# Kernel tuning notes

Hardware: AMD Instinct MI355X
Metric: run time of the kernel (lower is better)

Reference implementation:

```python
import jax, jax.numpy as jnp
import numpy as np

N_NODES = 16000
N_EDGES = 256000
F = 128        # invariant edge feature dim
MUL = 64       # multiplicity of env/V irreps (mul_gcd)
HID = 128      # mlp_n_hidden
SQRT3 = float(np.sqrt(3.0))

# e3nn-style activation normalization constant for silu:
# c = sqrt(E_{z~N(0,1)}[silu(z)^2]), so silu(z)/c has unit second moment.
_z = np.linspace(-12.0, 12.0, 100001)
_pdf = np.exp(-0.5 * _z ** 2) / np.sqrt(2.0 * np.pi)
_silu = _z / (1.0 + np.exp(-_z))
SILU_C = float(np.sqrt(np.trapz(_silu ** 2 * _pdf, _z)))


def _nsilu(x):
    return jax.nn.silu(x) / SILU_C


def _lin(x, W):
    # e3nn 'path' gradient normalization: W ~ N(0,1), forward scaled by 1/sqrt(fan_in)
    return (x @ W) / jnp.sqrt(jnp.asarray(W.shape[0], x.dtype))


def setup_inputs() -> dict:
    key = jax.random.key(0)
    ks = jax.random.split(key, 11)
    inp = {
        'vectors': jax.random.normal(ks[0], (N_EDGES, 3), jnp.float32),
        'x': jax.random.normal(ks[1], (N_EDGES, F), jnp.float32),
        'V': jax.random.normal(ks[2], (N_EDGES, 4 * MUL), jnp.float32),  # 64x0e + 64x1o
        'u': jax.random.uniform(ks[3], (N_EDGES,), jnp.float32),
        'm': jnp.ones((N_EDGES,), jnp.float32),
        'W_env': jax.random.normal(ks[4], (F, 2 * MUL), jnp.float32),
        'W1': jax.random.normal(ks[5], (F + 2 * MUL, HID), jnp.float32),
        'W2': jax.random.normal(ks[6], (HID, HID), jnp.float32),
        'W3': jax.random.normal(ks[7], (HID, HID), jnp.float32),
        'W_out': jax.random.normal(ks[8], (2 * MUL, MUL), jnp.float32),
        'senders': jax.random.randint(ks[9], (N_EDGES,), 0, N_NODES, jnp.int32),
    }
    return inp


def reference(vectors, x, V, u, m, W_env, W1, W2, W3, W_out, senders):
    E = vectors.shape[0]
    x = x * m[:, None]

    # n_neighbors = scatter_sum(m, dst=senders, map_back=True)
    n_neighbors = jax.ops.segment_sum(m, senders, num_segments=N_NODES)[senders]  # (E,)

    # w = Linear(num_irreps=2*MUL)(x)
    w = _lin(x, W_env)                  # (E, 128)
    w0, w1 = w[:, :MUL], w[:, MUL:]     # scalar / vector channel weights

    # spherical harmonics (component normalization): Y0 = 1, Y1 = sqrt(3)*rhat
    rhat = vectors / jnp.linalg.norm(vectors, axis=-1, keepdims=True)
    Y1 = SQRT3 * rhat                   # (E, 3)

    # w * Y * m, scatter_sum over senders, map back, normalize by n_neighbors
    denom = n_neighbors + 1e-5
    ws = w0 * m[:, None]                                   # (E, MUL)   w * Y0
    wv = (w1[:, :, None] * Y1[:, None, :]) * m[:, None, None]  # (E, MUL, 3)
    wY_s = jax.ops.segment_sum(ws, senders, num_segments=N_NODES)[senders] / denom[:, None]
    wY_v = jax.ops.segment_sum(wv, senders, num_segments=N_NODES)[senders] / denom[:, None, None]

    # V.mul_to_axis(): (E, MUL, 0e+1o)
    Vs = V[:, :MUL]                      # (E, MUL)
    Vv = V[:, MUL:].reshape(E, MUL, 3)   # (E, MUL, 3)

    # tensor product, filter_ir_out = {0e, 1o} (CG, component normalization)
    s_a = wY_s * Vs                                  # 0e x 0e -> 0e
    s_b = jnp.sum(wY_v * Vv, axis=-1) / SQRT3        # 1o x 1o -> 0e
    v_a = wY_s[:, :, None] * Vv                      # 0e x 1o -> 1o
    v_b = wY_v * Vs[:, :, None]                      # 1o x 0e -> 1o

    # scalars -> concatenated into x; vectors stay equivariant
    x = jnp.concatenate([x, s_a, s_b], axis=1)       # (E, F + 2*MUL)

    # invariant MLP (silu, no output activation)
    h = _nsilu(_lin(x, W1))
    h = _nsilu(_lin(h, W2))
    h = _lin(h, W3)                                  # (E, HID)
    x_out = u[:, None] * h

    # Linear(irreps_out=64x1o) on 128x1o
    V_in = jnp.concatenate([v_a, v_b], axis=1)       # (E, 2*MUL, 3)
    V_out = jnp.einsum('euk,uo->eok', V_in, W_out) / jnp.sqrt(jnp.asarray(2 * MUL, V.dtype))
    V_out = V_out.reshape(E, MUL * 3)                # (E, 192)

    return x_out, V_out
```

## Files before the change

kernel.cpp:

```cpp
#include <hip/hip_runtime.h>
#include <math.h>

typedef short bf16x8 __attribute__((ext_vector_type(8)));
typedef float f32x4 __attribute__((ext_vector_type(4)));

#define S128 0.08838834764831845f
#define S256I 0.0625f
#define NN_NODES 16000

#define WS_COUNTS   16448000
#define WS_OFFSETS  (WS_COUNTS + 64000)
#define WS_CURSOR   (WS_OFFSETS + 64000)
#define WS_INV      (WS_CURSOR + 64000)
#define WS_W1 (WS_INV + 1024000)
#define WS_W2 (WS_W1 + 65536)
#define WS_W3 (WS_W2 + 32768)
#define WS_WO (WS_W3 + 32768)
#define WS_WE (WS_WO + 16384)
#define WS_VECM (WS_WE + 32768)
#define WS_XMB  (WS_VECM + 4096000)

static float compute_inv_silu_c() {
    double sum = 0.0, prev = 0.0;
    const double dz = 24.0 / 100000.0;
    for (int i = 0; i <= 100000; ++i) {
        double z = -12.0 + dz * (double)i;
        double pdf = exp(-0.5 * z * z) * 0.3989422804014327;
        double s = z / (1.0 + exp(-z));
        double f = s * s * pdf;
        if (i) sum += 0.5 * (prev + f) * dz;
        prev = f;
    }
    return (float)(1.0 / sqrt(sum));
}
static const float INV_SILU_C = compute_inv_silu_c();

__device__ __forceinline__ unsigned int packbf(float a, float b) {
    union { float f; unsigned int u; } ca, cb;
    ca.f = a; cb.f = b;
    unsigned int ua = ca.u + (0x7fffu + ((ca.u >> 16) & 1u));
    unsigned int ub = cb.u + (0x7fffu + ((cb.u >> 16) & 1u));
    return (ua >> 16) | (ub & 0xffff0000u);
}
__device__ __forceinline__ unsigned short bf16r(float v) {
    union { float f; unsigned int u; } c; c.f = v;
    return (unsigned short)((c.u + (0x7fffu + ((c.u >> 16) & 1u))) >> 16);
}
__device__ __forceinline__ float bflo(unsigned int u) { return __uint_as_float(u << 16); }
__device__ __forceinline__ float bfhi(unsigned int u) { return __uint_as_float(u & 0xffff0000u); }
__device__ __forceinline__ int swz(int row, int b) { return b ^ ((row & 7) << 4); }
__device__ __forceinline__ float nsilu(float v, float ic) {
    return v / (1.0f + __expf(-v)) * ic;
}

__global__ __launch_bounds__(256) void k_wprep(
    const float* __restrict__ W1, const float* __restrict__ W2,
    const float* __restrict__ W3, const float* __restrict__ Wout,
    const float* __restrict__ Wenv, char* __restrict__ wsb)
{
    const int t = blockIdx.x * 256 + threadIdx.x;
    if (t < NN_NODES) ((int*)(wsb + WS_COUNTS))[t] = 0;
    if (t < 32768) {
        int n = t & 127, k = t >> 7;
        *(unsigned short*)(wsb + WS_W1 + n * 512 + k * 2) =
            bf16r(W1[k * 128 + n] * S256I);
    }
    if (t < 16384) {
        int n = t & 127, k = t >> 7;
        *(unsigned short*)(wsb + WS_W2 + n * 256 + k * 2) =
            bf16r(W2[k * 128 + n] * S128);
        *(unsigned short*)(wsb + WS_W3 + n * 256 + k * 2) =
            bf16r(W3[k * 128 + n] * S128);
    }
    if (t < 16384) {
        int j = t & 127, k = t >> 7;
        int c = (j & 1) ? 64 + (j >> 1) : (j >> 1);
        *(unsigned short*)(wsb + WS_WE + j * 256 + k * 2) =
            bf16r(Wenv[k * 128 + c] * S128);
    }
    if (t < 8192) {
        int o = t & 63, uu = t >> 6;
        *(unsigned short*)(wsb + WS_WO + o * 256 + ((uu * 2) ^ ((o & 7) << 4))) =
            bf16r(Wout[uu * 64 + o] * S128);
    }
}

__global__ __launch_bounds__(1024) void k_hist(
    const int* __restrict__ senders, int* __restrict__ counts, int E)
{
    const int e = blockIdx.x * 1024 + threadIdx.x;
    if (e < E) atomicAdd(&counts[senders[e]], 1);
}

__global__ __launch_bounds__(1024) void k_scan(
    const int* __restrict__ counts, int* __restrict__ offsets,
    int* __restrict__ cursor)
{
    __shared__ int part[1024];
    const int t = threadIdx.x;
    const int s0 = t * 16;
    const int s1 = (s0 + 16 < NN_NODES) ? s0 + 16 : NN_NODES;
    int s = 0;
    for (int i = s0; i < s1; ++i) s += counts[i];
    part[t] = s;
    __syncthreads();
    for (int off = 1; off < 1024; off <<= 1) {
        int v = part[t];
        if (t >= off) v += part[t - off];
        __syncthreads();
        part[t] = v;
        __syncthreads();
    }
    int run = t ? part[t - 1] : 0;
    for (int i = s0; i < s1; ++i) {
        offsets[i] = run; cursor[i] = run; run += counts[i];
    }
}

__global__ __launch_bounds__(1024) void k_binfill(
    const int* __restrict__ senders, const float* __restrict__ vectors,
    const float* __restrict__ m, int* __restrict__ cursor,
    int* __restrict__ inv, float4* __restrict__ vecm, int E)
{
    const int e = blockIdx.x * 1024 + threadIdx.x;
    if (e < E) {
        const int p = atomicAdd(&cursor[senders[e]], 1);
        inv[e] = p;
        float4 vm;
        vm.x = vectors[(size_t)e * 3 + 0];
        vm.y = vectors[(size_t)e * 3 + 1];
        vm.z = vectors[(size_t)e * 3 + 2];
        vm.w = m[e];
        vecm[p] = vm;
    }
}

__global__ __launch_bounds__(512) void k_env(
    const float* __restrict__ x, const float* __restrict__ m,
    const char* __restrict__ wsb, const int* __restrict__ inv,
    char* __restrict__ wout, char* __restrict__ xmb, int E)
{
    __shared__ char lds[32768];
    const int tid = threadIdx.x, l = tid & 63, wid = tid >> 6;
    const int lr = l & 15, lg = l >> 4;
    const int n0 = wid * 16;

    bf16x8 B[4];
    #pragma unroll
    for (int kk = 0; kk < 4; ++kk)
        B[kk] = *(const bf16x8*)(wsb + WS_WE + (n0 + lr) * 256 + kk * 64 + lg * 16);

    const int eb = blockIdx.x * 128;
    {
        const int el = tid >> 2, q = tid & 3;
        const int e = eb + el;
        if (e < E) {
            const float mv = m[e];
            const float4* xp = (const float4*)&x[(size_t)e * 128 + q * 32];
            #pragma unroll
            for (int j = 0; j < 4; ++j) {
                float4 A = xp[2 * j], Bv = xp[2 * j + 1];
                int4 w;
                w.x = packbf(A.x * mv, A.y * mv); w.y = packbf(A.z * mv, A.w * mv);
                w.z = packbf(Bv.x * mv, Bv.y * mv); w.w = packbf(Bv.z * mv, Bv.w * mv);
                *(int4*)(lds + el * 256 + swz(el, q * 64 + j * 16)) = w;
            }
        } else {
            const int4 z = {0, 0, 0, 0};
            #pragma unroll
            for (int j = 0; j < 4; ++j)
                *(int4*)(lds + el * 256 + swz(el, q * 64 + j * 16)) = z;
        }
    }
    __syncthreads();

    {
        const int el = tid >> 2, q = tid & 3;
        const int e = eb + el;
        if (e < E) {
            int4* d = (int4*)(xmb + (size_t)e * 256 + q * 64);
            #pragma unroll
            for (int j = 0; j < 4; ++j)
                d[j] = *(int4*)(lds + el * 256 + ((q * 64 + j * 16) ^ ((el & 7) << 4)));
        }
    }

    f32x4 acc[8];
    #pragma unroll
    for (int a = 0; a < 8; ++a) acc[a] = (f32x4){0.f, 0.f, 0.f, 0.f};

    #pragma unroll
    for (int kk = 0; kk < 4; ++kk) {
        const int kb = kk * 64 + lg * 16;
        #pragma unroll
        for (int mt = 0; mt < 8; ++mt) {
            const int row = mt * 16 + lr;
            bf16x8 a = *(const bf16x8*)(lds + row * 256 + swz(row, kb));
            acc[mt] = __builtin_amdgcn_mfma_f32_16x16x32_bf16(a, B[kk], acc[mt], 0, 0, 0);
        }
    }
    __syncthreads();

    #pragma unroll
    for (int mt = 0; mt < 8; ++mt)
        #pragma unroll
        for (int r = 0; r < 4; ++r) {
            const int row = mt * 16 + lg * 4 + r;
            *(unsigned short*)(lds + row * 256 + (((n0 + lr) * 2) ^ ((row & 7) << 4))) =
                bf16r(acc[mt][r]);
        }
    __syncthreads();

    {
        const int el = tid >> 2, q = tid & 3;
        const int e = eb + el;
        if (e < E) {
            const int p = inv[e];
            int4* d = (int4*)(wout + (size_t)p * 256 + q * 64);
            #pragma unroll
            for (int j = 0; j < 4; ++j)
                d[j] = *(int4*)(lds + el * 256 + ((q * 64 + j * 16) ^ ((el & 7) << 4)));
        }
    }
}

__global__ __launch_bounds__(256) void k_gather(
    const char* __restrict__ wvb, const float4* __restrict__ vecm,
    const int* __restrict__ counts, const int* __restrict__ offsets,
    float* __restrict__ node_cnt, float* __restrict__ node_s,
    float* __restrict__ node_v)
{
    const int l = threadIdx.x & 63, wid = threadIdx.x >> 6;
    const int n = blockIdx.x * 4 + wid;
    if (n >= NN_NODES) return;
    const int cnt = counts[n], base = offsets[n];

    float as = 0.f, a0 = 0.f, a1 = 0.f, a2 = 0.f, am = 0.f;
    for (int i = 0; i < cnt; ++i) {
        const unsigned int wv =
            *(const unsigned int*)(wvb + (size_t)(base + i) * 256 + l * 4);
        const float4 vm = vecm[base + i];
        const float rn = 1.7320508075688772f /
                         sqrtf(vm.x * vm.x + vm.y * vm.y + vm.z * vm.z);
        const float w0 = bflo(wv) * vm.w;
        const float c1 = bfhi(wv) * vm.w * rn;
        as += w0; am += vm.w;
        a0 += c1 * vm.x; a1 += c1 * vm.y; a2 += c1 * vm.z;
    }
    if (l == 0) node_cnt[n] = am;
    node_s[(size_t)n * 64 + l] = as;
    float* nv = &node_v[((size_t)n * 64 + l) * 3];
    nv[0] = a0; nv[1] = a1; nv[2] = a2;
}

__global__ __launch_bounds__(512) void k_prep_vout(
    const float* __restrict__ V, const int* __restrict__ senders,
    const float* __restrict__ node_cnt, const float* __restrict__ node_s,
    const float* __restrict__ node_v, const char* __restrict__ wsb,
    float* __restrict__ out_x, float* __restrict__ out_v, int E)
{
    __shared__ char lds[49152 + 16384];
    const int tid = threadIdx.x, l = tid & 63, wid = tid >> 6;

    {
        const int4* src = (const int4*)(wsb + WS_WO);
        int4 a = src[tid * 2], b = src[tid * 2 + 1];
        ((int4*)(lds + 49152))[tid * 2]     = a;
        ((int4*)(lds + 49152))[tid * 2 + 1] = b;
    }

    const int eb = blockIdx.x * 64;
    #pragma unroll 2
    for (int i = 0; i < 8; ++i) {
        const int el = wid * 8 + i;
        const int e  = eb + el;
        float Vs = 0.f, Vv0 = 0.f, Vv1 = 0.f, Vv2 = 0.f;
        float wYs = 0.f, wv0 = 0.f, wv1 = 0.f, wv2 = 0.f;
        if (e < E) {
            Vs = V[(size_t)e * 256 + l];
            const float* vp = &V[(size_t)e * 256 + 64 + l * 3];
            Vv0 = vp[0]; Vv1 = vp[1]; Vv2 = vp[2];
            const int sn = senders[e];
            const float rden = 1.0f / (node_cnt[sn] + 1e-5f);
            wYs = node_s[(size_t)sn * 64 + l] * rden;
            const float* nvp = &node_v[((size_t)sn * 64 + l) * 3];
            wv0 = nvp[0] * rden; wv1 = nvp[1] * rden; wv2 = nvp[2] * rden;
            unsigned short* sab = (unsigned short*)((char*)out_x + (size_t)e * 512);
            sab[l]      = bf16r(wYs * Vs);
            sab[64 + l] = bf16r((wv0 * Vv0 + wv1 * Vv1 + wv2 * Vv2) * 0.57735026918962576f);
        }
        const float vvk[3] = {Vv0, Vv1, Vv2};
        const float wvk[3] = {wv0, wv1, wv2};
        #pragma unroll
        for (int k = 0; k < 3; ++k) {
            const int row = el * 3 + k;
            *(unsigned short*)(lds + row * 256 + swz(row, l * 2))       = bf16r(wYs * vvk[k]);
            *(unsigned short*)(lds + row * 256 + swz(row, 128 + l * 2)) = bf16r(wvk[k] * Vs);
        }
    }
    __syncthreads();

    const int wm = wid & 3, wn = wid >> 2;
    const int m0 = wm * 48, n0 = wn * 32;
    const int lr = l & 15, lg = l >> 4;
    f32x4 acc[3][2];
    #pragma unroll
    for (int a = 0; a < 3; ++a)
        #pragma unroll
        for (int b = 0; b < 2; ++b) acc[a][b] = (f32x4){0.f, 0.f, 0.f, 0.f};

    #pragma unroll
    for (int kk = 0; kk < 4; ++kk) {
        const int kb = kk * 64 + lg * 16;
        bf16x8 a0 = *(const bf16x8*)(lds + (m0 + lr) * 256      + swz(m0 + lr, kb));
        bf16x8 a1 = *(const bf16x8*)(lds + (m0 + 16 + lr) * 256 + swz(m0 + 16 + lr, kb));
        bf16x8 a2 = *(const bf16x8*)(lds + (m0 + 32 + lr) * 256 + swz(m0 + 32 + lr, kb));
        bf16x8 b0 = *(const bf16x8*)(lds + 49152 + (n0 + lr) * 256      + swz(n0 + lr, kb));
        bf16x8 b1 = *(const bf16x8*)(lds + 49152 + (n0 + 16 + lr) * 256 + swz(n0 + 16 + lr, kb));
        acc[0][0] = __builtin_amdgcn_mfma_f32_16x16x32_bf16(a0, b0, acc[0][0], 0, 0, 0);
        acc[0][1] = __builtin_amdgcn_mfma_f32_16x16x32_bf16(a0, b1, acc[0][1], 0, 0, 0);
        acc[1][0] = __builtin_amdgcn_mfma_f32_16x16x32_bf16(a1, b0, acc[1][0], 0, 0, 0);
        acc[1][1] = __builtin_amdgcn_mfma_f32_16x16x32_bf16(a1, b1, acc[1][1], 0, 0, 0);
        acc[2][0] = __builtin_amdgcn_mfma_f32_16x16x32_bf16(a2, b0, acc[2][0], 0, 0, 0);
        acc[2][1] = __builtin_amdgcn_mfma_f32_16x16x32_bf16(a2, b1, acc[2][1], 0, 0, 0);
    }
    __syncthreads();

    #pragma unroll
    for (int mt = 0; mt < 3; ++mt)
        #pragma unroll
        for (int nt = 0; nt < 2; ++nt)
            #pragma unroll
            for (int r = 0; r < 4; ++r) {
                const int mm = m0 + mt * 16 + lg * 4 + r;
                const int el2 = mm / 3, kd = mm - el2 * 3;
                const int o = n0 + nt * 16 + lr;
                *(float*)(lds + el2 * 768 + (o * 3 + kd) * 4) = acc[mt][nt][r];
            }
    __syncthreads();
    if (eb + 64 <= E) {
        const int4* s = (const int4*)lds;
        int4* d = (int4*)(out_v + (size_t)eb * 192);
        #pragma unroll
        for (int j = 0; j < 6; ++j) d[tid * 6 + j] = s[tid * 6 + j];
    } else {
        for (int idx = tid; idx < 64 * 192; idx += 512) {
            const int el2 = idx / 192;
            if (eb + el2 < E)
                out_v[(size_t)(eb + el2) * 192 + (idx % 192)] = *(float*)(lds + idx * 4);
        }
    }
}

__global__ __launch_bounds__(512, 4) void k_mlp(
    const char* __restrict__ xmb, const float* __restrict__ ug,
    const char* __restrict__ wsb, float* __restrict__ out_x,
    float inv_c, int E)
{
    __shared__ char lds[49152];
    const int tid = threadIdx.x, l = tid & 63, wid = tid >> 6;
    const int lr = l & 15, lg = l >> 4;
    const int n0 = wid * 16;
    const int eb = blockIdx.x * 64;

    bf16x8 B1[8];
    #pragma unroll
    for (int kk = 0; kk < 8; ++kk)
        B1[kk] = *(const bf16x8*)(wsb + WS_W1 + (n0 + lr) * 512 + kk * 64 + lg * 16);

    {
        const int el = tid >> 3, q = tid & 7;
        const int e = eb + el;
        if (e < E) {
            const int4* xp = (const int4*)(xmb + (size_t)e * 256 + q * 32);
            *(int4*)(lds + el * 512 + swz(el, q * 32))      = xp[0];
            *(int4*)(lds + el * 512 + swz(el, q * 32 + 16)) = xp[1];
            const int4* sp = (const int4*)((const char*)out_x + (size_t)e * 512 + q * 32);
            *(int4*)(lds + el * 512 + swz(el, 256 + q * 32))      = sp[0];
            *(int4*)(lds + el * 512 + swz(el, 256 + q * 32 + 16)) = sp[1];
        } else {
            const int4 z = {0, 0, 0, 0};
            *(int4*)(lds + el * 512 + swz(el, q * 32))            = z;
            *(int4*)(lds + el * 512 + swz(el, q * 32 + 16))       = z;
            *(int4*)(lds + el * 512 + swz(el, 256 + q * 32))      = z;
            *(int4*)(lds + el * 512 + swz(el, 256 + q * 32 + 16)) = z;
        }
    }
    __syncthreads();

    f32x4 a1[4];
    #pragma unroll
    for (int a = 0; a < 4; ++a) a1[a] = (f32x4){0.f, 0.f, 0.f, 0.f};
    #pragma unroll
    for (int kk = 0; kk < 8; ++kk) {
        const int kb = kk * 64 + lg * 16;
        #pragma unroll
        for (int mt = 0; mt < 4; ++mt) {
            const int row = mt * 16 + lr;
            bf16x8 a = *(const bf16x8*)(lds + row * 512 + swz(row, kb));
            a1[mt] = __builtin_amdgcn_mfma_f32_16x16x32_bf16(a, B1[kk], a1[mt], 0, 0, 0);
        }
    }

    bf16x8 B2[4], B3[4];
    #pragma unroll
    for (int kk = 0; kk < 4; ++kk) {
        B2[kk] = *(const bf16x8*)(wsb + WS_W2 + (n0 + lr) * 256 + kk * 64 + lg * 16);
        B3[kk] = *(const bf16x8*)(wsb + WS_W3 + (n0 + lr) * 256 + kk * 64 + lg * 16);
    }

    #pragma unroll
    for (int mt = 0; mt < 4; ++mt)
        #pragma unroll
        for (int r = 0; r < 4; ++r) {
            const int row = mt * 16 + lg * 4 + r;
            *(unsigned short*)(lds + 32768 + row * 256 + swz(row, (n0 + lr) * 2)) =
                bf16r(nsilu(a1[mt][r], inv_c));
        }
    __syncthreads();

    f32x4 a2[4];
    #pragma unroll
    for (int a = 0; a < 4; ++a) a2[a] = (f32x4){0.f, 0.f, 0.f, 0.f};
    #pragma unroll
    for (int kk = 0; kk < 4; ++kk) {
        const int kb = kk * 64 + lg * 16;
        #pragma unroll
        for (int mt = 0; mt < 4; ++mt) {
            const int row = mt * 16 + lr;
            bf16x8 a = *(const bf16x8*)(lds + 32768 + row * 256 + swz(row, kb));
            a2[mt] = __builtin_amdgcn_mfma_f32_16x16x32_bf16(a, B2[kk], a2[mt], 0, 0, 0);
        }
    }
    #pragma unroll
    for (int mt = 0; mt < 4; ++mt)
        #pragma unroll
        for (int r = 0; r < 4; ++r) {
            const int row = mt * 16 + lg * 4 + r;
            *(unsigned short*)(lds + row * 256 + swz(row, (n0 + lr) * 2)) =
                bf16r(nsilu(a2[mt][r], inv_c));
        }
    __syncthreads();

    f32x4 a3[4];
    #pragma unroll
    for (int a = 0; a < 4; ++a) a3[a] = (f32x4){0.f, 0.f, 0.f, 0.f};
    #pragma unroll
    for (int kk = 0; kk < 4; ++kk) {
        const int kb = kk * 64 + lg * 16;
        #pragma unroll
        for (int mt = 0; mt < 4; ++mt) {
            const int row = mt * 16 + lr;
            bf16x8 a = *(const bf16x8*)(lds + row * 256 + swz(row, kb));
            a3[mt] = __builtin_amdgcn_mfma_f32_16x16x32_bf16(a, B3[kk], a3[mt], 0, 0, 0);
        }
    }
    __syncthreads();

    #pragma unroll
    for (int mt = 0; mt < 4; ++mt)
        #pragma unroll
        for (int r = 0; r < 4; ++r) {
            const int row = mt * 16 + lg * 4 + r;
            *(float*)(lds + row * 512 + (((n0 + lr) * 4) ^ ((row & 7) << 4))) = a3[mt][r];
        }
    __syncthreads();

    {
        const int el = tid >> 3, q = tid & 7;
        const int e = eb + el;
        if (e < E) {
            const float uu = ug[e];
            #pragma unroll
            for (int j = 0; j < 4; ++j) {
                int4 v = *(int4*)(lds + el * 512 + ((q * 64 + j * 16) ^ ((el & 7) << 4)));
                float4 f;
                f.x = __int_as_float(v.x) * uu; f.y = __int_as_float(v.y) * uu;
                f.z = __int_as_float(v.z) * uu; f.w = __int_as_float(v.w) * uu;
                *(float4*)(&out_x[(size_t)e * 128 + q * 16 + j * 4]) = f;
            }
        }
    }
}

extern "C" void kernel_launch(void* const* d_in, const int* in_sizes, int n_in,
                              void* d_out, int out_size, void* d_ws, size_t ws_size,
                              hipStream_t stream) {
    const float* vectors = (const float*)d_in[0];
    const float* x       = (const float*)d_in[1];
    const float* V       = (const float*)d_in[2];
    const float* u       = (const float*)d_in[3];
    const float* m       = (const float*)d_in[4];
    const float* W_env   = (const float*)d_in[5];
    const float* W1      = (const float*)d_in[6];
    const float* W2      = (const float*)d_in[7];
    const float* W3      = (const float*)d_in[8];
    const float* W_out   = (const float*)d_in[9];
    const int*   senders = (const int*)d_in[10];

    const int E = in_sizes[4];

    char*  wsb      = (char*)d_ws;
    float* node_cnt = (float*)d_ws;
    float* node_s   = node_cnt + NN_NODES;
    float* node_v   = node_s + (size_t)NN_NODES * 64;
    int* counts  = (int*)(wsb + WS_COUNTS);
    int* offsets = (int*)(wsb + WS_OFFSETS);
    int* cursor  = (int*)(wsb + WS_CURSOR);
    int* inv     = (int*)(wsb + WS_INV);
    float4* vecm = (float4*)(wsb + WS_VECM);
    char* xmb    = wsb + WS_XMB;

    float* out_x = (float*)d_out;
    float* out_v = out_x + (size_t)E * 128;
    char*  wvb   = (char*)out_v;

    k_wprep<<<128, 256, 0, stream>>>(W1, W2, W3, W_out, W_env, wsb);
    k_hist<<<(E + 1023) / 1024, 1024, 0, stream>>>(senders, counts, E);
    k_scan<<<1, 1024, 0, stream>>>(counts, offsets, cursor);
    k_binfill<<<(E + 1023) / 1024, 1024, 0, stream>>>(senders, vectors, m,
                                                      cursor, inv, vecm, E);
    k_env<<<(E + 127) / 128, 512, 0, stream>>>(x, m, wsb, inv, wvb, xmb, E);
    k_gather<<<(NN_NODES + 3) / 4, 256, 0, stream>>>(wvb, vecm, counts, offsets,
                                                     node_cnt, node_s, node_v);
    k_prep_vout<<<(E + 63) / 64, 512, 0, stream>>>(V, senders, node_cnt, node_s,
                                                   node_v, wsb, out_x, out_v, E);
    k_mlp<<<(E + 63) / 64, 512, 0, stream>>>(xmb, u, wsb, out_x, INV_SILU_C, E);
}
```

Measured before the change: 448.5 us.

## Fuse V-output prep and MLP kernels, keeping tensor-product scalars in LDS

```diff
diff --git a/kernel.cpp b/kernel.cpp
--- a/kernel.cpp
+++ b/kernel.cpp
@@ -253,20 +253,22 @@
     nv[0] = a0; nv[1] = a1; nv[2] = a2;
 }
 
-__global__ __launch_bounds__(512) void k_prep_vout(
+__global__ __launch_bounds__(512, 4) void k_fuse(
     const float* __restrict__ V, const int* __restrict__ senders,
     const float* __restrict__ node_cnt, const float* __restrict__ node_s,
     const float* __restrict__ node_v, const char* __restrict__ wsb,
-    float* __restrict__ out_x, float* __restrict__ out_v, int E)
-{
-    __shared__ char lds[49152 + 16384];
+    const char* __restrict__ xmb, const float* __restrict__ ug,
+    float* __restrict__ out_x, float* __restrict__ out_v,
+    float inv_c, int E)
+{
+    __shared__ char lds[81920];
     const int tid = threadIdx.x, l = tid & 63, wid = tid >> 6;
+    const int lr = l & 15, lg = l >> 4;
 
     {
         const int4* src = (const int4*)(wsb + WS_WO);
-        int4 a = src[tid * 2], b = src[tid * 2 + 1];
-        ((int4*)(lds + 49152))[tid * 2]     = a;
-        ((int4*)(lds + 49152))[tid * 2 + 1] = b;
+        ((int4*)(lds + 49152))[tid * 2]     = src[tid * 2];
+        ((int4*)(lds + 49152))[tid * 2 + 1] = src[tid * 2 + 1];
     }
 
     const int eb = blockIdx.x * 64;
@@ -285,10 +287,10 @@
             wYs = node_s[(size_t)sn * 64 + l] * rden;
             const float* nvp = &node_v[((size_t)sn * 64 + l) * 3];
             wv0 = nvp[0] * rden; wv1 = nvp[1] * rden; wv2 = nvp[2] * rden;
-            unsigned short* sab = (unsigned short*)((char*)out_x + (size_t)e * 512);
-            sab[l]      = bf16r(wYs * Vs);
-            sab[64 + l] = bf16r((wv0 * Vv0 + wv1 * Vv1 + wv2 * Vv2) * 0.57735026918962576f);
-        }
+        }
+        *(unsigned short*)(lds + 65536 + el * 256 + l * 2) = bf16r(wYs * Vs);
+        *(unsigned short*)(lds + 65536 + el * 256 + 128 + l * 2) =
+            bf16r((wv0 * Vv0 + wv1 * Vv1 + wv2 * Vv2) * 0.57735026918962576f);
         const float vvk[3] = {Vv0, Vv1, Vv2};
         const float wvk[3] = {wv0, wv1, wv2};
         #pragma unroll
@@ -300,43 +302,44 @@
     }
     __syncthreads();
 
-    const int wm = wid & 3, wn = wid >> 2;
-    const int m0 = wm * 48, n0 = wn * 32;
-    const int lr = l & 15, lg = l >> 4;
-    f32x4 acc[3][2];
-    #pragma unroll
-    for (int a = 0; a < 3; ++a)
-        #pragma unroll
-        for (int b = 0; b < 2; ++b) acc[a][b] = (f32x4){0.f, 0.f, 0.f, 0.f};
-
-    #pragma unroll
-    for (int kk = 0; kk < 4; ++kk) {
-        const int kb = kk * 64 + lg * 16;
-        bf16x8 a0 = *(const bf16x8*)(lds + (m0 + lr) * 256      + swz(m0 + lr, kb));
-        bf16x8 a1 = *(const bf16x8*)(lds + (m0 + 16 + lr) * 256 + swz(m0 + 16 + lr, kb));
-        bf16x8 a2 = *(const bf16x8*)(lds + (m0 + 32 + lr) * 256 + swz(m0 + 32 + lr, kb));
-        bf16x8 b0 = *(const bf16x8*)(lds + 49152 + (n0 + lr) * 256      + swz(n0 + lr, kb));
-        bf16x8 b1 = *(const bf16x8*)(lds + 49152 + (n0 + 16 + lr) * 256 + swz(n0 + 16 + lr, kb));
-        acc[0][0] = __builtin_amdgcn_mfma_f32_16x16x32_bf16(a0, b0, acc[0][0], 0, 0, 0);
-        acc[0][1] = __builtin_amdgcn_mfma_f32_16x16x32_bf16(a0, b1, acc[0][1], 0, 0, 0);
-        acc[1][0] = __builtin_amdgcn_mfma_f32_16x16x32_bf16(a1, b0, acc[1][0], 0, 0, 0);
-        acc[1][1] = __builtin_amdgcn_mfma_f32_16x16x32_bf16(a1, b1, acc[1][1], 0, 0, 0);
-        acc[2][0] = __builtin_amdgcn_mfma_f32_16x16x32_bf16(a2, b0, acc[2][0], 0, 0, 0);
-        acc[2][1] = __builtin_amdgcn_mfma_f32_16x16x32_bf16(a2, b1, acc[2][1], 0, 0, 0);
-    }
-    __syncthreads();
-
-    #pragma unroll
-    for (int mt = 0; mt < 3; ++mt)
-        #pragma unroll
-        for (int nt = 0; nt < 2; ++nt)
-            #pragma unroll
-            for (int r = 0; r < 4; ++r) {
-                const int mm = m0 + mt * 16 + lg * 4 + r;
-                const int el2 = mm / 3, kd = mm - el2 * 3;
-                const int o = n0 + nt * 16 + lr;
-                *(float*)(lds + el2 * 768 + (o * 3 + kd) * 4) = acc[mt][nt][r];
-            }
+    {
+        const int wm = wid & 3, wn = wid >> 2;
+        const int m0 = wm * 48, n0v = wn * 32;
+        f32x4 acc[3][2];
+        #pragma unroll
+        for (int a = 0; a < 3; ++a)
+            #pragma unroll
+            for (int b = 0; b < 2; ++b) acc[a][b] = (f32x4){0.f, 0.f, 0.f, 0.f};
+
+        #pragma unroll
+        for (int kk = 0; kk < 4; ++kk) {
+            const int kb = kk * 64 + lg * 16;
+            bf16x8 a0 = *(const bf16x8*)(lds + (m0 + lr) * 256      + swz(m0 + lr, kb));
+            bf16x8 a1 = *(const bf16x8*)(lds + (m0 + 16 + lr) * 256 + swz(m0 + 16 + lr, kb));
+            bf16x8 a2 = *(const bf16x8*)(lds + (m0 + 32 + lr) * 256 + swz(m0 + 32 + lr, kb));
+            bf16x8 b0 = *(const bf16x8*)(lds + 49152 + (n0v + lr) * 256      + swz(n0v + lr, kb));
+            bf16x8 b1 = *(const bf16x8*)(lds + 49152 + (n0v + 16 + lr) * 256 + swz(n0v + 16 + lr, kb));
+            acc[0][0] = __builtin_amdgcn_mfma_f32_16x16x32_bf16(a0, b0, acc[0][0], 0, 0, 0);
+            acc[0][1] = __builtin_amdgcn_mfma_f32_16x16x32_bf16(a0, b1, acc[0][1], 0, 0, 0);
+            acc[1][0] = __builtin_amdgcn_mfma_f32_16x16x32_bf16(a1, b0, acc[1][0], 0, 0, 0);
+            acc[1][1] = __builtin_amdgcn_mfma_f32_16x16x32_bf16(a1, b1, acc[1][1], 0, 0, 0);
+            acc[2][0] = __builtin_amdgcn_mfma_f32_16x16x32_bf16(a2, b0, acc[2][0], 0, 0, 0);
+            acc[2][1] = __builtin_amdgcn_mfma_f32_16x16x32_bf16(a2, b1, acc[2][1], 0, 0, 0);
+        }
+        __syncthreads();
+
+        #pragma unroll
+        for (int mt = 0; mt < 3; ++mt)
+            #pragma unroll
+            for (int nt = 0; nt < 2; ++nt)
+                #pragma unroll
+                for (int r = 0; r < 4; ++r) {
+                    const int mm = m0 + mt * 16 + lg * 4 + r;
+                    const int el2 = mm / 3, kd = mm - el2 * 3;
+                    const int o = n0v + nt * 16 + lr;
+                    *(float*)(lds + el2 * 768 + (o * 3 + kd) * 4) = acc[mt][nt][r];
+                }
+    }
     __syncthreads();
     if (eb + 64 <= E) {
         const int4* s = (const int4*)lds;
@@ -350,19 +353,9 @@
                 out_v[(size_t)(eb + el2) * 192 + (idx % 192)] = *(float*)(lds + idx * 4);
         }
     }
-}
-
-__global__ __launch_bounds__(512, 4) void k_mlp(
-    const char* __restrict__ xmb, const float* __restrict__ ug,
-    const char* __restrict__ wsb, float* __restrict__ out_x,
-    float inv_c, int E)
-{
-    __shared__ char lds[49152];
-    const int tid = threadIdx.x, l = tid & 63, wid = tid >> 6;
-    const int lr = l & 15, lg = l >> 4;
+    __syncthreads();
+
     const int n0 = wid * 16;
-    const int eb = blockIdx.x * 64;
-
     bf16x8 B1[8];
     #pragma unroll
     for (int kk = 0; kk < 8; ++kk)
@@ -371,20 +364,19 @@
     {
         const int el = tid >> 3, q = tid & 7;
         const int e = eb + el;
+        int4 x0, x1;
         if (e < E) {
             const int4* xp = (const int4*)(xmb + (size_t)e * 256 + q * 32);
-            *(int4*)(lds + el * 512 + swz(el, q * 32))      = xp[0];
-            *(int4*)(lds + el * 512 + swz(el, q * 32 + 16)) = xp[1];
-            const int4* sp = (const int4*)((const char*)out_x + (size_t)e * 512 + q * 32);
-            *(int4*)(lds + el * 512 + swz(el, 256 + q * 32))      = sp[0];
-            *(int4*)(lds + el * 512 + swz(el, 256 + q * 32 + 16)) = sp[1];
+            x0 = xp[0]; x1 = xp[1];
         } else {
-            const int4 z = {0, 0, 0, 0};
-            *(int4*)(lds + el * 512 + swz(el, q * 32))            = z;
-            *(int4*)(lds + el * 512 + swz(el, q * 32 + 16))       = z;
-            *(int4*)(lds + el * 512 + swz(el, 256 + q * 32))      = z;
-            *(int4*)(lds + el * 512 + swz(el, 256 + q * 32 + 16)) = z;
-        }
+            x0 = (int4){0, 0, 0, 0}; x1 = (int4){0, 0, 0, 0};
+        }
+        *(int4*)(lds + el * 512 + swz(el, q * 32))      = x0;
+        *(int4*)(lds + el * 512 + swz(el, q * 32 + 16)) = x1;
+        int4 s0 = *(int4*)(lds + 65536 + el * 256 + q * 32);
+        int4 s1 = *(int4*)(lds + 65536 + el * 256 + q * 32 + 16);
+        *(int4*)(lds + el * 512 + swz(el, 256 + q * 32))      = s0;
+        *(int4*)(lds + el * 512 + swz(el, 256 + q * 32 + 16)) = s1;
     }
     __syncthreads();
 
@@ -523,7 +515,7 @@
     k_env<<<(E + 127) / 128, 512, 0, stream>>>(x, m, wsb, inv, wvb, xmb, E);
     k_gather<<<(NN_NODES + 3) / 4, 256, 0, stream>>>(wvb, vecm, counts, offsets,
                                                      node_cnt, node_s, node_v);
-    k_prep_vout<<<(E + 63) / 64, 512, 0, stream>>>(V, senders, node_cnt, node_s,
-                                                   node_v, wsb, out_x, out_v, E);
-    k_mlp<<<(E + 63) / 64, 512, 0, stream>>>(xmb, u, wsb, out_x, INV_SILU_C, E);
-}
+    k_fuse<<<(E + 63) / 64, 512, 0, stream>>>(V, senders, node_cnt, node_s,
+                                              node_v, wsb, xmb, u,
+                                              out_x, out_v, INV_SILU_C, E);
+}
```

Result: no change. 439.8 us (-1.9%).
